# Kernel tuning notes

Measured on AMD Instinct MI355X. Metric: run time of the kernel, lower is better.

Reference implementation:

```python
import jax, jax.numpy as jnp
import numpy as np

NUM_HEADS = 8


def setup_inputs() -> dict:
    key = jax.random.key(0)
    ks = jax.random.split(key, 7)
    B, H, W, C = 1, 64, 64, 512
    x = jax.random.normal(ks[0], (B, H, W, C), dtype=jnp.float32)
    # lat in [-pi/2, pi/2), lon in [0, 2*pi) radians
    lat_grid = (jax.random.uniform(ks[1], (H, W), dtype=jnp.float32) - 0.5) * np.float32(np.pi)
    lon_grid = jax.random.uniform(ks[2], (H, W), dtype=jnp.float32) * np.float32(2 * np.pi)
    w_qkv = jax.random.normal(ks[3], (3 * C, C), dtype=jnp.float32) * 0.02
    b_qkv = jax.random.normal(ks[4], (3 * C,), dtype=jnp.float32) * 0.02
    w_out = jax.random.normal(ks[5], (C, C), dtype=jnp.float32) * 0.02
    b_out = jax.random.normal(ks[6], (C,), dtype=jnp.float32) * 0.02
    return {"x": x, "lat_grid": lat_grid, "lon_grid": lon_grid,
            "w_qkv": w_qkv, "b_qkv": b_qkv, "w_out": w_out, "b_out": b_out}


def _distance_bias(lat_grid, lon_grid):
    # Haversine great-circle distance between all pairs of grid points.
    lat = lat_grid.reshape(-1)  # [N]
    lon = lon_grid.reshape(-1)
    dlat = lat[None, :] - lat[:, None]  # [N, N]
    dlon = lon[None, :] - lon[:, None]
    a = jnp.sin(dlat / 2) ** 2 + jnp.cos(lat)[:, None] * jnp.cos(lat)[None, :] * jnp.sin(dlon / 2) ** 2
    dist = 2.0 * jnp.arcsin(jnp.sqrt(jnp.clip(a, 0.0, 1.0)))
    # torch .std() is unbiased (ddof=1)
    return -dist / jnp.std(dist, ddof=1)


def reference(x, lat_grid, lon_grid, w_qkv, b_qkv, w_out, b_out):
    B, H, W, C = x.shape
    nh = NUM_HEADS
    dh = C // nh
    N = H * W
    qkv = x @ w_qkv.T + b_qkv  # [B, H, W, 3C]
    qkv = qkv.reshape(B, N, 3, nh, dh)
    q = jnp.transpose(qkv[:, :, 0], (0, 2, 1, 3))  # [B, nh, N, dh]
    k = jnp.transpose(qkv[:, :, 1], (0, 2, 1, 3))
    v = jnp.transpose(qkv[:, :, 2], (0, 2, 1, 3))
    scale = np.float32(1.0 / np.sqrt(dh))
    attn = jnp.einsum("bhnd,bhmd->bhnm", q, k) * scale  # [B, nh, N, N]
    attn = attn + _distance_bias(lat_grid, lon_grid)[None, None]
    attn = jax.nn.softmax(attn, axis=-1)  # dropout is identity in eval
    out = jnp.einsum("bhnm,bhmd->bhnd", attn, v)  # [B, nh, N, dh]
    out = jnp.transpose(out, (0, 2, 1, 3)).reshape(B, H, W, C)
    return out @ w_out.T + b_out
```

## Files before the change

kernel.cpp:

```cpp
#include <hip/hip_runtime.h>
#include <hip/hip_bf16.h>


typedef __attribute__((ext_vector_type(8))) short bf16x8;
typedef __attribute__((ext_vector_type(4))) float f32x4;

#define MFMA16(a, b, c) __builtin_amdgcn_mfma_f32_16x16x32_bf16(a, b, c, 0, 0, 0)

__device__ __forceinline__ unsigned short f2b(float f) {
    union { float f; unsigned int i; } v;
    v.f = f;
    unsigned int lsb = (v.i >> 16) & 1u;
    unsigned int r = v.i + 0x7fffu + lsb;
    return (unsigned short)(r >> 16);
}

__global__ __launch_bounds__(256) void prep_kernel(
    const float* __restrict__ lat, const float* __restrict__ lon,
    float* __restrict__ dist, double* __restrict__ partials,
    const float* __restrict__ x, unsigned short* __restrict__ xb,
    const float* __restrict__ wq, unsigned short* __restrict__ wqb,
    const float* __restrict__ wo, unsigned short* __restrict__ wob) {
    __shared__ float sl_i[64], sc_i[64], so_i[64];
    __shared__ float sl_j[64], sc_j[64], so_j[64];
    __shared__ double rs[256], rs2[256];

    int b = blockIdx.x;
    int tid = threadIdx.x;

    if (b < 4096) {
        int i0 = (b >> 6) << 6;
        int j0 = (b & 63) << 6;

        if (tid < 64) {
            float la = lat[i0 + tid];
            sl_i[tid] = la; sc_i[tid] = __cosf(la); so_i[tid] = lon[i0 + tid];
        } else if (tid < 128) {
            int t = tid - 64;
            float la = lat[j0 + t];
            sl_j[t] = la; sc_j[t] = __cosf(la); so_j[t] = lon[j0 + t];
        }
        __syncthreads();

        float s = 0.f, s2 = 0.f;
        int col = tid & 63;
        int colpart = ((col >> 4) << 8) + (((col >> 2) & 3) << 6) + (col & 3);
        size_t tbase = ((size_t)(j0 >> 6) << 10) + colpart;
        float latj = sl_j[col], cj = sc_j[col], lonj = so_j[col];
#pragma unroll
        for (int kk = 0; kk < 16; kk++) {
            int row = (kk << 2) + (tid >> 6);
            float dlat = latj - sl_i[row];
            float dlon = lonj - so_i[row];
            float h1 = __sinf(0.5f * dlat);
            float h2 = __sinf(0.5f * dlon);
            float a = h1 * h1 + sc_i[row] * cj * h2 * h2;
            a = fminf(fmaxf(a, 0.0f), 1.0f);
            float d = 2.0f * asinf(sqrtf(a));
            dist[tbase + ((size_t)((i0 >> 4) + (row >> 4)) << 16)
                 + ((row & 15) << 2)] = d;
            s += d;
            s2 += d * d;
        }
        rs[tid] = (double)s; rs2[tid] = (double)s2;
        __syncthreads();
        for (int off = 128; off > 0; off >>= 1) {
            if (tid < off) { rs[tid] += rs[tid + off]; rs2[tid] += rs2[tid + off]; }
            __syncthreads();
        }
        if (tid == 0) {
            partials[2 * b] = rs[0];
            partials[2 * b + 1] = rs2[0];
        }
        return;
    }

    const float* in; unsigned short* out; int t;
    if (b < 5120)      { in = x;  out = xb;  t = (b - 4096) * 256 + tid; }
    else if (b < 5504) { in = wq; out = wqb; t = (b - 5120) * 256 + tid; }
    else               { in = wo; out = wob; t = (b - 5504) * 256 + tid; }
    int l = t & 15, qd = (t >> 4) & 3, c = (t >> 6) & 15, g = t >> 10;
    const float* src = in + ((size_t)g * 16 + l) * 512 + c * 32 + qd * 8;
    float4 v0 = *(const float4*)src;
    float4 v1 = *(const float4*)(src + 4);
    ushort4 u0, u1;
    u0.x = f2b(v0.x); u0.y = f2b(v0.y); u0.z = f2b(v0.z); u0.w = f2b(v0.w);
    u1.x = f2b(v1.x); u1.y = f2b(v1.y); u1.z = f2b(v1.z); u1.w = f2b(v1.w);
    unsigned short* dst = out + (size_t)t * 8;
    *(ushort4*)dst = u0;
    *(ushort4*)(dst + 4) = u1;
}

__global__ __launch_bounds__(256) void qkv_gemm(
    const unsigned short* __restrict__ x, const unsigned short* __restrict__ w,
    const float* __restrict__ b,
    unsigned short* __restrict__ q, unsigned short* __restrict__ k,
    unsigned short* __restrict__ vt,
    const double* __restrict__ partials, float* __restrict__ neg_inv_std) {
    __shared__ unsigned short stage[64][72];
    __shared__ double rs[256], rs2[256];
    int lane = threadIdx.x & 63, wave = threadIdx.x >> 6;
    int l16 = lane & 15, quad = lane >> 4;

    if (blockIdx.x == 24) {
        if (blockIdx.y != 0) return;
        int tid = threadIdx.x;
        double s = 0.0, s2 = 0.0;
        for (int i = tid; i < 4096; i += 256) {
            s += partials[2 * i];
            s2 += partials[2 * i + 1];
        }
        rs[tid] = s; rs2[tid] = s2;
        __syncthreads();
        for (int off = 128; off > 0; off >>= 1) {
            if (tid < off) { rs[tid] += rs[tid + off]; rs2[tid] += rs2[tid + off]; }
            __syncthreads();
        }
        if (tid == 0) {
            double n = 16777216.0;
            double mean = rs[0] / n;
            double var = (rs2[0] - n * mean * mean) / (n - 1.0);
            *neg_inv_std = (float)(-1.0 / sqrt(var));
        }
        return;
    }

    int m0 = blockIdx.y * 64 + wave * 16;
    int n0 = blockIdx.x * 64;

    const unsigned short* abase = x + (size_t)(blockIdx.y * 4 + wave) * 8192 + lane * 8;
    f32x4 acc[4];
#pragma unroll
    for (int nb = 0; nb < 4; nb++) acc[nb] = (f32x4){0.f, 0.f, 0.f, 0.f};

    for (int k0 = 0; k0 < 512; k0 += 32) {
        bf16x8 af = *(const bf16x8*)(abase + (k0 >> 5) * 512);
#pragma unroll
        for (int nb = 0; nb < 4; nb++) {
            bf16x8 bf = *(const bf16x8*)(w + (size_t)((n0 >> 4) + nb) * 8192
                                           + (k0 >> 5) * 512 + lane * 8);
            acc[nb] = MFMA16(af, bf, acc[nb]);
        }
    }
    if (blockIdx.x < 8) {
#pragma unroll
        for (int nb = 0; nb < 4; nb++) {
            int j = n0 + nb * 16 + l16;
            float bj = b[j];
            int h = j >> 6, d = j & 63;
#pragma unroll
            for (int r = 0; r < 4; r++) {
                int n = m0 + quad * 4 + r;
                q[((size_t)h * 4096 + n) * 64 + d] = f2b((acc[nb][r] + bj) * 0.125f);
            }
        }
    } else if (blockIdx.x < 16) {
        int h = blockIdx.x - 8;
#pragma unroll
        for (int nb = 0; nb < 4; nb++) {
            int d = nb * 16 + l16;
            float bj = b[512 + h * 64 + d];
#pragma unroll
            for (int r = 0; r < 4; r++)
                stage[wave * 16 + quad * 4 + r][d] = f2b(acc[nb][r] + bj);
        }
        __syncthreads();
        unsigned short* kb = k + ((size_t)h << 18) + (size_t)blockIdx.y * 4096;
#pragma unroll
        for (int p = 0; p < 2; p++) {
            int rid = p * 256 + threadIdx.x;
            int t = rid >> 7;
            int rem = rid & 127;
            int half = rem >> 6, qd = (rem >> 4) & 3, l = rem & 15;
            const unsigned short* src = &stage[t * 16 + l][half * 32 + qd * 8];
            unsigned short* dst = kb + t * 1024 + half * 512 + qd * 128 + l * 8;
            *(uint4*)dst = *(const uint4*)src;
        }
    } else {
        int h = blockIdx.x - 16;
#pragma unroll
        for (int nb = 0; nb < 4; nb++) {
            int d = nb * 16 + l16;
            float bj = b[1024 + h * 64 + d];
#pragma unroll
            for (int r = 0; r < 4; r++)
                stage[d][quad * 8 + (wave & 1) * 4 + r + (wave >> 1) * 32] =
                    f2b(acc[nb][r] + bj);
        }
        __syncthreads();
        int t = threadIdx.x;
        int d = t >> 2;
        int nq = (t & 3) * 16;
        unsigned short* dst = vt + ((size_t)h << 18) + (size_t)blockIdx.y * 4096
                            + (d >> 4) * 1024 + ((nq >> 5) & 1) * 512
                            + ((nq >> 3) & 3) * 128 + (d & 15) * 8;
        const unsigned short* src = &stage[d][nq];
        *(uint4*)dst = *(const uint4*)src;
        *(uint4*)(dst + 128) = *(const uint4*)(src + 8);
    }
}

__device__ __forceinline__ void attn_step(
    const unsigned short* __restrict__ kptr, const unsigned short* __restrict__ vtp,
    int h, int kv0, int lane,
    bf16x8 qf0, bf16x8 qf1, f32x4 (&dv)[4], const float* __restrict__ dbase,
    int kv_next, float nis, f32x4 (&o)[4], float& lam) {
    size_t tbase = ((size_t)h << 18) + ((size_t)kv0 << 6) + lane * 8;
    const unsigned short* kb = kptr + tbase;
    const unsigned short* vb = vtp + tbase;
    f32x4 s[4];
    __builtin_amdgcn_s_setprio(1);
#pragma unroll
    for (int cb = 0; cb < 4; cb++) {
        bf16x8 kf0 = *(const bf16x8*)(kb + cb * 1024);
        bf16x8 kf1 = *(const bf16x8*)(kb + cb * 1024 + 512);
        f32x4 z = (f32x4){0.f, 0.f, 0.f, 0.f};
        z = MFMA16(kf0, qf0, z);
        z = MFMA16(kf1, qf1, z);
        s[cb] = z;
    }
    __builtin_amdgcn_s_setprio(0);
    bf16x8 vf[8];
#pragma unroll
    for (int db = 0; db < 4; db++) {
        vf[2 * db]     = *(const bf16x8*)(vb + db * 1024);
        vf[2 * db + 1] = *(const bf16x8*)(vb + db * 1024 + 512);
    }
#pragma unroll
    for (int cb = 0; cb < 4; cb++) {
        s[cb][0] = fmaf(dv[cb][0], nis, s[cb][0]);
        s[cb][1] = fmaf(dv[cb][1], nis, s[cb][1]);
        s[cb][2] = fmaf(dv[cb][2], nis, s[cb][2]);
        s[cb][3] = fmaf(dv[cb][3], nis, s[cb][3]);
    }
    {
        const float* dnext = dbase + ((size_t)(kv_next >> 6) << 10);
#pragma unroll
        for (int cb = 0; cb < 4; cb++)
            dv[cb] = *(const f32x4*)(dnext + cb * 256);
    }
    bf16x8 pf0, pf1;
#pragma unroll
    for (int cb = 0; cb < 4; cb++) {
        float p0 = __expf(s[cb][0]);
        float p1 = __expf(s[cb][1]);
        float p2 = __expf(s[cb][2]);
        float p3 = __expf(s[cb][3]);
        lam += (p0 + p1) + (p2 + p3);
        if (cb < 2) {
            pf0[cb * 4 + 0] = (short)f2b(p0);
            pf0[cb * 4 + 1] = (short)f2b(p1);
            pf0[cb * 4 + 2] = (short)f2b(p2);
            pf0[cb * 4 + 3] = (short)f2b(p3);
        } else {
            pf1[(cb - 2) * 4 + 0] = (short)f2b(p0);
            pf1[(cb - 2) * 4 + 1] = (short)f2b(p1);
            pf1[(cb - 2) * 4 + 2] = (short)f2b(p2);
            pf1[(cb - 2) * 4 + 3] = (short)f2b(p3);
        }
    }
    __builtin_amdgcn_s_setprio(1);
#pragma unroll
    for (int db = 0; db < 4; db++) {
        o[db] = MFMA16(pf0, vf[2 * db], o[db]);
        o[db] = MFMA16(pf1, vf[2 * db + 1], o[db]);
    }
    __builtin_amdgcn_s_setprio(0);
}

__global__ __launch_bounds__(512, 4) void attn_kernel(
    const unsigned short* __restrict__ q, const unsigned short* __restrict__ k,
    const unsigned short* __restrict__ vt, const float* __restrict__ dist,
    const float* __restrict__ nis_p, unsigned short* __restrict__ att) {
    __shared__ __align__(16) char smem[8704];
    int tid = threadIdx.x;
    int lane = tid & 63, wave = tid >> 6;
    int l16 = lane & 15, quad = lane >> 4;
    int b = blockIdx.x;
    int xcd = b & 7, j = b >> 3;
    int h  = (xcd & 3) * 2 + (j & 1);
    int qs = (xcd >> 2) * 64 + (j >> 1);
    int qgl = wave & 1;
    int qt = wave >> 1;
    int q0 = qs * 32 + qgl * 16;
    int kvbase = qt * 1024;
    float nis = *nis_p;

    const unsigned short* qbase = q + ((size_t)h * 4096 + q0 + l16) * 64 + quad * 8;
    bf16x8 qf0 = *(const bf16x8*)(qbase);
    bf16x8 qf1 = *(const bf16x8*)(qbase + 32);

    f32x4 o[4];
    float lam = 0.f;
#pragma unroll
    for (int r = 0; r < 4; r++) {
        o[0][r] = 0.f; o[1][r] = 0.f; o[2][r] = 0.f; o[3][r] = 0.f;
    }

    const float* dbase = dist + ((size_t)(q0 >> 4) << 16) + quad * 64 + l16 * 4;
    f32x4 dv[4];
    {
        const float* d0 = dbase + ((size_t)(kvbase >> 6) << 10);
#pragma unroll
        for (int cb = 0; cb < 4; cb++)
            dv[cb] = *(const f32x4*)(d0 + cb * 256);
    }

    for (int it = 0; it < 16; ++it) {
        int kv0 = kvbase + it * 64;
        int kvn = (it == 15) ? kvbase : kv0 + 64;
        attn_step(k, vt, h, kv0, lane, qf0, qf1, dv, dbase, kvn, nis, o, lam);
    }

    lam += __shfl_xor(lam, 16, 64);
    lam += __shfl_xor(lam, 32, 64);

    __syncthreads();
    float* obuf = (float*)smem;
    float* lbuf = (float*)(smem + 8192);
    if (lane < 16)
        lbuf[qt * 32 + qgl * 16 + lane] = lam;
    if (qt == 0) {
#pragma unroll
        for (int db = 0; db < 4; db++)
#pragma unroll
            for (int r = 0; r < 4; r++)
                obuf[(qgl * 16 + quad * 4 + r) * 64 + db * 16 + l16] = o[db][r];
    }
    __syncthreads();
    if (qt == 1) {
#pragma unroll
        for (int db = 0; db < 4; db++)
#pragma unroll
            for (int r = 0; r < 4; r++)
                obuf[(qgl * 16 + quad * 4 + r) * 64 + db * 16 + l16] += o[db][r];
    }
    __syncthreads();
    if (qt == 2) {
#pragma unroll
        for (int db = 0; db < 4; db++)
#pragma unroll
            for (int r = 0; r < 4; r++)
                obuf[(qgl * 16 + quad * 4 + r) * 64 + db * 16 + l16] += o[db][r];
    }
    __syncthreads();
    if (qt == 3) {
#pragma unroll
        for (int db = 0; db < 4; db++)
#pragma unroll
            for (int r = 0; r < 4; r++)
                obuf[(qgl * 16 + quad * 4 + r) * 64 + db * 16 + l16] += o[db][r];
    }
    __syncthreads();

    int rl = tid >> 4;
    int d4 = (tid & 15) * 4;
    float L = lbuf[rl] + lbuf[32 + rl] + lbuf[64 + rl] + lbuf[96 + rl];
    float rinv = 1.0f / L;
    const float* ob = obuf + rl * 64 + d4;
    ushort4 ua;
    ua.x = f2b(ob[0] * rinv); ua.y = f2b(ob[1] * rinv);
    ua.z = f2b(ob[2] * rinv); ua.w = f2b(ob[3] * rinv);
    int row = qs * 32 + rl;
    int col = h * 64 + d4;
    size_t dst = (size_t)(row >> 4) * 8192 + (col >> 5) * 512
               + ((col >> 3) & 3) * 128 + (row & 15) * 8 + (col & 7);
    *(ushort4*)(att + dst) = ua;
}

__global__ __launch_bounds__(256) void out_gemm(
    const unsigned short* __restrict__ att, const unsigned short* __restrict__ w,
    const float* __restrict__ b, float* __restrict__ out) {
    int lane = threadIdx.x & 63, wave = threadIdx.x >> 6;
    int l16 = lane & 15, quad = lane >> 4;
    int m0 = blockIdx.y * 64 + wave * 16;
    int n0 = blockIdx.x * 64;

    const unsigned short* abase = att + (size_t)(blockIdx.y * 4 + wave) * 8192 + lane * 8;
    f32x4 acc[4];
#pragma unroll
    for (int nb = 0; nb < 4; nb++) acc[nb] = (f32x4){0.f, 0.f, 0.f, 0.f};

    for (int k0 = 0; k0 < 512; k0 += 32) {
        bf16x8 af = *(const bf16x8*)(abase + (k0 >> 5) * 512);
#pragma unroll
        for (int nb = 0; nb < 4; nb++) {
            bf16x8 bf = *(const bf16x8*)(w + (size_t)((n0 >> 4) + nb) * 8192
                                           + (k0 >> 5) * 512 + lane * 8);
            acc[nb] = MFMA16(af, bf, acc[nb]);
        }
    }
#pragma unroll
    for (int nb = 0; nb < 4; nb++) {
        float bj = b[n0 + nb * 16 + l16];
#pragma unroll
        for (int r = 0; r < 4; r++)
            out[(size_t)(m0 + quad * 4 + r) * 512 + n0 + nb * 16 + l16] =
                acc[nb][r] + bj;
    }
}

extern "C" void kernel_launch(void* const* d_in, const int* in_sizes, int n_in,
                              void* d_out, int out_size, void* d_ws, size_t ws_size,
                              hipStream_t stream) {
    const float* x    = (const float*)d_in[0];
    const float* lat  = (const float*)d_in[1];
    const float* lon  = (const float*)d_in[2];
    const float* wqkv = (const float*)d_in[3];
    const float* bqkv = (const float*)d_in[4];
    const float* wout = (const float*)d_in[5];
    const float* bout = (const float*)d_in[6];
    float* out = (float*)d_out;

    char* ws = (char*)d_ws;
    float* dist        = (float*)ws;
    double* partials   = (double*)(ws + 67108864);
    float* nis         = (float*)(ws + 67108864 + 65536);
    unsigned short* q  = (unsigned short*)(ws + 67108864 + 65600);
    unsigned short* k  = q  + (size_t)8 * 4096 * 64;
    unsigned short* vt = k  + (size_t)8 * 4096 * 64;
    unsigned short* att = vt + (size_t)8 * 4096 * 64;
    unsigned short* xb  = att + (size_t)4096 * 512;
    unsigned short* wqb = xb  + (size_t)4096 * 512;
    unsigned short* wob = wqb + (size_t)1536 * 512;

    prep_kernel<<<5632, 256, 0, stream>>>(lat, lon, dist, partials,
                                          x, xb, wqkv, wqb, wout, wob);
    qkv_gemm<<<dim3(25, 64), 256, 0, stream>>>(xb, wqb, bqkv, q, k, vt,
                                               partials, nis);
    attn_kernel<<<1024, 512, 0, stream>>>(q, k, vt, dist, nis, att);
    out_gemm<<<dim3(8, 64), 256, 0, stream>>>(att, wob, bout, out);
}
```

Before: 218.8 us.

## Co-schedule distance-bias computation with QKV GEMM in one launch

Splits the bf16 conversion into its own small kernel and merges the haversine distance/partial-sum blocks with the QKV projection GEMM blocks into a single grid. The final std reduction moves to a dedicated one-block kernel. The aim is to overlap the compute-bound transcendental distance work with the MFMA GEMM so that neither leaves the GPU underused. This adds one extra kernel launch, and the mixed block types share one shared-memory footprint, which may reduce occupancy.

```diff
diff --git a/kernel.cpp b/kernel.cpp
--- a/kernel.cpp
+++ b/kernel.cpp
@@ -15,22 +15,46 @@
     return (unsigned short)(r >> 16);
 }
 
-__global__ __launch_bounds__(256) void prep_kernel(
-    const float* __restrict__ lat, const float* __restrict__ lon,
-    float* __restrict__ dist, double* __restrict__ partials,
+__global__ __launch_bounds__(256) void cvt_kernel(
     const float* __restrict__ x, unsigned short* __restrict__ xb,
     const float* __restrict__ wq, unsigned short* __restrict__ wqb,
     const float* __restrict__ wo, unsigned short* __restrict__ wob) {
+    int b = blockIdx.x, tid = threadIdx.x;
+    const float* in; unsigned short* out; int t;
+    if (b < 1024)      { in = x;  out = xb;  t = b * 256 + tid; }
+    else if (b < 1408) { in = wq; out = wqb; t = (b - 1024) * 256 + tid; }
+    else               { in = wo; out = wob; t = (b - 1408) * 256 + tid; }
+    int l = t & 15, qd = (t >> 4) & 3, c = (t >> 6) & 15, g = t >> 10;
+    const float* src = in + ((size_t)g * 16 + l) * 512 + c * 32 + qd * 8;
+    float4 v0 = *(const float4*)src;
+    float4 v1 = *(const float4*)(src + 4);
+    ushort4 u0, u1;
+    u0.x = f2b(v0.x); u0.y = f2b(v0.y); u0.z = f2b(v0.z); u0.w = f2b(v0.w);
+    u1.x = f2b(v1.x); u1.y = f2b(v1.y); u1.z = f2b(v1.z); u1.w = f2b(v1.w);
+    unsigned short* dst = out + (size_t)t * 8;
+    *(ushort4*)dst = u0;
+    *(ushort4*)(dst + 4) = u1;
+}
+
+__global__ __launch_bounds__(256) void dist_qkv_kernel(
+    const float* __restrict__ lat, const float* __restrict__ lon,
+    float* __restrict__ dist, double* __restrict__ partials,
+    const unsigned short* __restrict__ x, const unsigned short* __restrict__ w,
+    const float* __restrict__ b,
+    unsigned short* __restrict__ q, unsigned short* __restrict__ k,
+    unsigned short* __restrict__ vt) {
+    __shared__ unsigned short stage[64][72];
     __shared__ float sl_i[64], sc_i[64], so_i[64];
     __shared__ float sl_j[64], sc_j[64], so_j[64];
     __shared__ double rs[256], rs2[256];
 
-    int b = blockIdx.x;
+    int blk = blockIdx.x;
     int tid = threadIdx.x;
 
-    if (b < 4096) {
-        int i0 = (b >> 6) << 6;
-        int j0 = (b & 63) << 6;
+    if (blk >= 1536) {
+        int db = blk - 1536;
+        int i0 = (db >> 6) << 6;
+        int j0 = (db & 63) << 6;
 
         if (tid < 64) {
             float la = lat[i0 + tid];
@@ -69,66 +93,20 @@
             __syncthreads();
         }
         if (tid == 0) {
-            partials[2 * b] = rs[0];
-            partials[2 * b + 1] = rs2[0];
+            partials[2 * db] = rs[0];
+            partials[2 * db + 1] = rs2[0];
         }
         return;
     }
 
-    const float* in; unsigned short* out; int t;
-    if (b < 5120)      { in = x;  out = xb;  t = (b - 4096) * 256 + tid; }
-    else if (b < 5504) { in = wq; out = wqb; t = (b - 5120) * 256 + tid; }
-    else               { in = wo; out = wob; t = (b - 5504) * 256 + tid; }
-    int l = t & 15, qd = (t >> 4) & 3, c = (t >> 6) & 15, g = t >> 10;
-    const float* src = in + ((size_t)g * 16 + l) * 512 + c * 32 + qd * 8;
-    float4 v0 = *(const float4*)src;
-    float4 v1 = *(const float4*)(src + 4);
-    ushort4 u0, u1;
-    u0.x = f2b(v0.x); u0.y = f2b(v0.y); u0.z = f2b(v0.z); u0.w = f2b(v0.w);
-    u1.x = f2b(v1.x); u1.y = f2b(v1.y); u1.z = f2b(v1.z); u1.w = f2b(v1.w);
-    unsigned short* dst = out + (size_t)t * 8;
-    *(ushort4*)dst = u0;
-    *(ushort4*)(dst + 4) = u1;
-}
-
-__global__ __launch_bounds__(256) void qkv_gemm(
-    const unsigned short* __restrict__ x, const unsigned short* __restrict__ w,
-    const float* __restrict__ b,
-    unsigned short* __restrict__ q, unsigned short* __restrict__ k,
-    unsigned short* __restrict__ vt,
-    const double* __restrict__ partials, float* __restrict__ neg_inv_std) {
-    __shared__ unsigned short stage[64][72];
-    __shared__ double rs[256], rs2[256];
-    int lane = threadIdx.x & 63, wave = threadIdx.x >> 6;
+    int by = blk / 24;
+    int bx = blk - by * 24;
+    int lane = tid & 63, wave = tid >> 6;
     int l16 = lane & 15, quad = lane >> 4;
-
-    if (blockIdx.x == 24) {
-        if (blockIdx.y != 0) return;
-        int tid = threadIdx.x;
-        double s = 0.0, s2 = 0.0;
-        for (int i = tid; i < 4096; i += 256) {
-            s += partials[2 * i];
-            s2 += partials[2 * i + 1];
-        }
-        rs[tid] = s; rs2[tid] = s2;
-        __syncthreads();
-        for (int off = 128; off > 0; off >>= 1) {
-            if (tid < off) { rs[tid] += rs[tid + off]; rs2[tid] += rs2[tid + off]; }
-            __syncthreads();
-        }
-        if (tid == 0) {
-            double n = 16777216.0;
-            double mean = rs[0] / n;
-            double var = (rs2[0] - n * mean * mean) / (n - 1.0);
-            *neg_inv_std = (float)(-1.0 / sqrt(var));
-        }
-        return;
-    }
-
-    int m0 = blockIdx.y * 64 + wave * 16;
-    int n0 = blockIdx.x * 64;
-
-    const unsigned short* abase = x + (size_t)(blockIdx.y * 4 + wave) * 8192 + lane * 8;
+    int m0 = by * 64 + wave * 16;
+    int n0 = bx * 64;
+
+    const unsigned short* abase = x + (size_t)(by * 4 + wave) * 8192 + lane * 8;
     f32x4 acc[4];
 #pragma unroll
     for (int nb = 0; nb < 4; nb++) acc[nb] = (f32x4){0.f, 0.f, 0.f, 0.f};
@@ -142,20 +120,20 @@
             acc[nb] = MFMA16(af, bf, acc[nb]);
         }
     }
-    if (blockIdx.x < 8) {
+    if (bx < 8) {
 #pragma unroll
         for (int nb = 0; nb < 4; nb++) {
-            int j = n0 + nb * 16 + l16;
-            float bj = b[j];
-            int h = j >> 6, d = j & 63;
+            int jj = n0 + nb * 16 + l16;
+            float bj = b[jj];
+            int h = jj >> 6, d = jj & 63;
 #pragma unroll
             for (int r = 0; r < 4; r++) {
                 int n = m0 + quad * 4 + r;
                 q[((size_t)h * 4096 + n) * 64 + d] = f2b((acc[nb][r] + bj) * 0.125f);
             }
         }
-    } else if (blockIdx.x < 16) {
-        int h = blockIdx.x - 8;
+    } else if (bx < 16) {
+        int h = bx - 8;
 #pragma unroll
         for (int nb = 0; nb < 4; nb++) {
             int d = nb * 16 + l16;
@@ -165,10 +143,10 @@
                 stage[wave * 16 + quad * 4 + r][d] = f2b(acc[nb][r] + bj);
         }
         __syncthreads();
-        unsigned short* kb = k + ((size_t)h << 18) + (size_t)blockIdx.y * 4096;
+        unsigned short* kb = k + ((size_t)h << 18) + (size_t)by * 4096;
 #pragma unroll
         for (int p = 0; p < 2; p++) {
-            int rid = p * 256 + threadIdx.x;
+            int rid = p * 256 + tid;
             int t = rid >> 7;
             int rem = rid & 127;
             int half = rem >> 6, qd = (rem >> 4) & 3, l = rem & 15;
@@ -177,7 +155,7 @@
             *(uint4*)dst = *(const uint4*)src;
         }
     } else {
-        int h = blockIdx.x - 16;
+        int h = bx - 16;
 #pragma unroll
         for (int nb = 0; nb < 4; nb++) {
             int d = nb * 16 + l16;
@@ -188,15 +166,38 @@
                     f2b(acc[nb][r] + bj);
         }
         __syncthreads();
-        int t = threadIdx.x;
+        int t = tid;
         int d = t >> 2;
         int nq = (t & 3) * 16;
-        unsigned short* dst = vt + ((size_t)h << 18) + (size_t)blockIdx.y * 4096
+        unsigned short* dst = vt + ((size_t)h << 18) + (size_t)by * 4096
                             + (d >> 4) * 1024 + ((nq >> 5) & 1) * 512
                             + ((nq >> 3) & 3) * 128 + (d & 15) * 8;
         const unsigned short* src = &stage[d][nq];
         *(uint4*)dst = *(const uint4*)src;
         *(uint4*)(dst + 128) = *(const uint4*)(src + 8);
+    }
+}
+
+__global__ __launch_bounds__(256) void stats_kernel(
+    const double* __restrict__ partials, float* __restrict__ neg_inv_std) {
+    __shared__ double rs[256], rs2[256];
+    int tid = threadIdx.x;
+    double s = 0.0, s2 = 0.0;
+    for (int i = tid; i < 4096; i += 256) {
+        s += partials[2 * i];
+        s2 += partials[2 * i + 1];
+    }
+    rs[tid] = s; rs2[tid] = s2;
+    __syncthreads();
+    for (int off = 128; off > 0; off >>= 1) {
+        if (tid < off) { rs[tid] += rs[tid + off]; rs2[tid] += rs2[tid + off]; }
+        __syncthreads();
+    }
+    if (tid == 0) {
+        double n = 16777216.0;
+        double mean = rs[0] / n;
+        double var = (rs2[0] - n * mean * mean) / (n - 1.0);
+        *neg_inv_std = (float)(-1.0 / sqrt(var));
     }
 }
 
@@ -424,10 +425,10 @@
     unsigned short* wqb = xb  + (size_t)4096 * 512;
     unsigned short* wob = wqb + (size_t)1536 * 512;
 
-    prep_kernel<<<5632, 256, 0, stream>>>(lat, lon, dist, partials,
-                                          x, xb, wqkv, wqb, wout, wob);
-    qkv_gemm<<<dim3(25, 64), 256, 0, stream>>>(xb, wqb, bqkv, q, k, vt,
-                                               partials, nis);
+    cvt_kernel<<<1536, 256, 0, stream>>>(x, xb, wqkv, wqb, wout, wob);
+    dist_qkv_kernel<<<5632, 256, 0, stream>>>(lat, lon, dist, partials,
+                                              xb, wqb, bqkv, q, k, vt);
+    stats_kernel<<<1, 256, 0, stream>>>(partials, nis);
     attn_kernel<<<1024, 512, 0, stream>>>(q, k, vt, dist, nis, att);
     out_gemm<<<dim3(8, 64), 256, 0, stream>>>(att, wob, bout, out);
 }
```

Result: no change. 221.3 us (+1.1%).
